# Kernel tuning notes

Measured on AMD Instinct MI355X. Metric: run time of the kernel, lower is better.

Reference implementation:

```python
import jax, jax.numpy as jnp
import numpy as np

SQ, SK, D = 8192, 8192, 128

def setup_inputs() -> dict:
    k = jax.random.key(0)
    kq, kk, kv = jax.random.split(k, 3)
    query = jax.random.normal(kq, (SQ, D), dtype=jnp.float32)
    key = jax.random.normal(kk, (SK, D), dtype=jnp.float32)
    value = jax.random.normal(kv, (SK, D), dtype=jnp.float32)
    return {"query": query, "key": key, "value": value}

def reference(query, key, value):
    # attn_weights = dot_general(q, k, contract last dims) -> [Sq, Sk]
    attn_weights = jnp.einsum('qd,kd->qk', query, key)
    # softmax over key dims (second half of attn_weights dims)
    attn_weights = jax.nn.softmax(attn_weights, axis=-1)
    # dropout is identity: train=False -> deterministic
    # y = dot_general(attn_weights, value, contract key dims) -> [Sq, Dv]
    y = jnp.einsum('qk,kd->qd', attn_weights, value)
    return y
```

## Files before the change

kernel.cpp:

```cpp
#include <hip/hip_runtime.h>
#include <hip/hip_bf16.h>
#include <stdint.h>

#define SQ 8192
#define SK 8192
#define DH 128
#define NIT 32
#define L2E 1.4426950408889634f
#define CB 40.0f

typedef __attribute__((ext_vector_type(8))) _Float16 f16x8;
typedef __attribute__((ext_vector_type(8))) short bf16x8;
typedef __attribute__((ext_vector_type(16))) float f32x16;
typedef __attribute__((ext_vector_type(4))) short s16x4;
typedef __attribute__((ext_vector_type(4))) unsigned int u32x4;

__device__ __forceinline__ short f2h(float f) {
  _Float16 h = (_Float16)f;
  return __builtin_bit_cast(short, h);
}
__device__ __forceinline__ short f2bf(float f) {
  uint32_t u = __builtin_bit_cast(uint32_t, f);
  u = (u + 0x7FFFu + ((u >> 16) & 1u)) >> 16;
  return (short)u;
}

__device__ __forceinline__ void gl_lds16(const void* g, void* l) {
  __builtin_amdgcn_global_load_lds(
      (const __attribute__((address_space(1))) void*)g,
      (__attribute__((address_space(3))) void*)l, 16, 0, 0);
}

__global__ __launch_bounds__(256) void prep_kernel(const float* __restrict__ K,
                                                   const float* __restrict__ V,
                                                   short* __restrict__ Kimg,
                                                   short* __restrict__ Vimg) {
  __shared__ short T[32][136];
  const int tid = threadIdx.x;
  if (blockIdx.x < 256) {
    const int kb = blockIdx.x;
#pragma unroll
    for (int i = 0; i < 2; ++i) {
      int ci = i * 256 + tid;
      int kc = ci >> 6, lane = ci & 63;
      int key = kb * 32 + (lane & 31);
      int k0 = kc * 16 + (lane >> 5) * 8;
      const float* src = K + (size_t)key * DH + k0;
      float4 a = *(const float4*)src;
      float4 b = *(const float4*)(src + 4);
      s16x4 o0, o1;
      o0.x = f2h(a.x); o0.y = f2h(a.y); o0.z = f2h(a.z); o0.w = f2h(a.w);
      o1.x = f2h(b.x); o1.y = f2h(b.y); o1.z = f2h(b.z); o1.w = f2h(b.w);
      s16x4* dst = (s16x4*)(Kimg + (size_t)kb * 4096 + ci * 8);
      dst[0] = o0; dst[1] = o1;
    }
  } else {
    const int kb = blockIdx.x - 256;
#pragma unroll
    for (int i = 0; i < 4; ++i) {
      int fi = i * 256 + tid;
      int key = fi >> 5;
      int dc = (fi & 31) * 4;
      float4 v = ((const float4*)V)[(size_t)(kb * 32 + key) * (DH / 4) + (fi & 31)];
      T[key][dc + 0] = f2bf(v.x); T[key][dc + 1] = f2bf(v.y);
      T[key][dc + 2] = f2bf(v.z); T[key][dc + 3] = f2bf(v.w);
    }
    __syncthreads();
#pragma unroll
    for (int i = 0; i < 2; ++i) {
      int ci = i * 256 + tid;
      int lane = ci & 63;
      int g = ci >> 6;
      int dt = g & 3, ks = g >> 2;
      int base = ks * 16 + (lane >> 5) * 4;
      int d = dt * 32 + (lane & 31);
      s16x4 o0, o1;
      o0.x = T[base + 0][d]; o0.y = T[base + 1][d];
      o0.z = T[base + 2][d]; o0.w = T[base + 3][d];
      o1.x = T[base + 8][d]; o1.y = T[base + 9][d];
      o1.z = T[base + 10][d]; o1.w = T[base + 11][d];
      s16x4* dst = (s16x4*)(Vimg + (size_t)kb * 4096 + ci * 8);
      dst[0] = o0; dst[1] = o1;
    }
  }
}

__global__ __launch_bounds__(512, 2) void attn_fallback(const float* __restrict__ Q,
                                                        const short* __restrict__ Kimg,
                                                        const short* __restrict__ Vimg,
                                                        float* __restrict__ out) {
  __shared__ __align__(16) char smem[67584];
  const int tid = threadIdx.x;
  const int w = tid >> 6;
  const int lane = tid & 63;
  const int half = lane >> 5;
  const int l32 = lane & 31;
  const int qrow0 = blockIdx.x * 32;

  f16x8 qf[8];
  {
    const float* qp = Q + (size_t)(qrow0 + l32) * DH + half * 8;
#pragma unroll
    for (int kc = 0; kc < 8; ++kc) {
      float4 a = *(const float4*)(qp + kc * 16);
      float4 b = *(const float4*)(qp + kc * 16 + 4);
      f16x8 h;
      h[0] = (_Float16)a.x; h[1] = (_Float16)a.y; h[2] = (_Float16)a.z; h[3] = (_Float16)a.w;
      h[4] = (_Float16)b.x; h[5] = (_Float16)b.y; h[6] = (_Float16)b.z; h[7] = (_Float16)b.w;
      qf[kc] = h;
    }
  }

  f32x16 of[4];
#pragma unroll
  for (int dt = 0; dt < 4; ++dt)
#pragma unroll
    for (int c = 0; c < 16; ++c) of[dt][c] = 0.f;
  float l_lane = 0.f;

  f16x8 kf[8];
  bf16x8 vf[8];
  {
    const short* kp = Kimg + (size_t)w * 4096;
    const short* vp = Vimg + (size_t)w * 4096;
#pragma unroll
    for (int kc = 0; kc < 8; ++kc) kf[kc] = *(const f16x8*)(kp + kc * 512 + lane * 8);
#pragma unroll
    for (int g = 0; g < 8; ++g) vf[g] = *(const bf16x8*)(vp + g * 512 + lane * 8);
  }

  for (int t = 0; t < NIT; ++t) {
    f32x16 sacc;
#pragma unroll
    for (int c = 0; c < 16; ++c) sacc[c] = 0.f;
#pragma unroll
    for (int kc = 0; kc < 8; ++kc)
      sacc = __builtin_amdgcn_mfma_f32_32x32x16_f16(kf[kc], qf[kc], sacc, 0, 0, 0);

    if (t + 1 < NIT) {
      const short* kp = Kimg + (size_t)((t + 1) * 8 + w) * 4096;
#pragma unroll
      for (int kc = 0; kc < 8; ++kc) kf[kc] = *(const f16x8*)(kp + kc * 512 + lane * 8);
    }

    u32x4 pav0, pav1;
#pragma unroll
    for (int r = 0; r < 4; ++r) {
      float pA = __builtin_amdgcn_exp2f(fmaf(sacc[2 * r], L2E, -CB));
      float pB = __builtin_amdgcn_exp2f(fmaf(sacc[2 * r + 1], L2E, -CB));
      float pC = __builtin_amdgcn_exp2f(fmaf(sacc[8 + 2 * r], L2E, -CB));
      float pD = __builtin_amdgcn_exp2f(fmaf(sacc[8 + 2 * r + 1], L2E, -CB));
      l_lane += (pA + pB) + (pC + pD);
      uint32_t uA = __builtin_bit_cast(uint32_t, pA); uA += 0x7FFFu + ((uA >> 16) & 1u);
      uint32_t uB = __builtin_bit_cast(uint32_t, pB); uB += 0x7FFFu + ((uB >> 16) & 1u);
      uint32_t uC = __builtin_bit_cast(uint32_t, pC); uC += 0x7FFFu + ((uC >> 16) & 1u);
      uint32_t uD = __builtin_bit_cast(uint32_t, pD); uD += 0x7FFFu + ((uD >> 16) & 1u);
      pav0[r] = __builtin_amdgcn_perm(uB, uA, 0x07060302u);
      pav1[r] = __builtin_amdgcn_perm(uD, uC, 0x07060302u);
    }
    bf16x8 pa0 = __builtin_bit_cast(bf16x8, pav0);
    bf16x8 pa1 = __builtin_bit_cast(bf16x8, pav1);

#pragma unroll
    for (int dt = 0; dt < 4; ++dt) {
      of[dt] = __builtin_amdgcn_mfma_f32_32x32x16_bf16(pa0, vf[dt], of[dt], 0, 0, 0);
      of[dt] = __builtin_amdgcn_mfma_f32_32x32x16_bf16(pa1, vf[4 + dt], of[dt], 0, 0, 0);
    }

    if (t + 1 < NIT) {
      const short* vp = Vimg + (size_t)((t + 1) * 8 + w) * 4096;
#pragma unroll
      for (int g = 0; g < 8; ++g) vf[g] = *(const bf16x8*)(vp + g * 512 + lane * 8);
    }
  }

  float l_tot = l_lane + __shfl_xor(l_lane, 32);

  __syncthreads();
  float* mO = (float*)smem;
  float* R = mO + (w & 3) * 4224;
  if (w < 4) {
#pragma unroll
    for (int c = 0; c < 16; ++c) {
      const int row = (c & 3) + 8 * (c >> 2) + 4 * half;
      float* br = R + row * 132;
#pragma unroll
      for (int dt = 0; dt < 4; ++dt) br[dt * 32 + l32] = of[dt][c];
    }
    if (half == 0) R[l32 * 132 + 128] = l_tot;
  }
  __syncthreads();
  if (w >= 4) {
#pragma unroll
    for (int c = 0; c < 16; ++c) {
      const int row = (c & 3) + 8 * (c >> 2) + 4 * half;
      float* br = R + row * 132;
#pragma unroll
      for (int dt = 0; dt < 4; ++dt) br[dt * 32 + l32] += of[dt][c];
    }
    if (half == 0) R[l32 * 132 + 128] += l_tot;
  }
  __syncthreads();
  {
    const int row = tid >> 4;
    const int cg = tid & 15;
    float den = mO[row * 132 + 128] + mO[4224 + row * 132 + 128] +
                mO[8448 + row * 132 + 128] + mO[12672 + row * 132 + 128];
    float inv = 1.f / den;
    float4 s0 = {0.f, 0.f, 0.f, 0.f}, s1 = {0.f, 0.f, 0.f, 0.f};
#pragma unroll
    for (int rg = 0; rg < 4; ++rg) {
      const float* p = mO + rg * 4224 + row * 132 + cg * 8;
      float4 a = *(const float4*)p;
      float4 b = *(const float4*)(p + 4);
      s0.x += a.x; s0.y += a.y; s0.z += a.z; s0.w += a.w;
      s1.x += b.x; s1.y += b.y; s1.z += b.z; s1.w += b.w;
    }
    s0.x *= inv; s0.y *= inv; s0.z *= inv; s0.w *= inv;
    s1.x *= inv; s1.y *= inv; s1.z *= inv; s1.w *= inv;
    float* op = out + (size_t)(qrow0 + row) * DH + cg * 8;
    *(float4*)op = s0;
    *(float4*)(op + 4) = s1;
  }
}

__global__ __launch_bounds__(512, 2) void attn_split(const float* __restrict__ Q,
                                                     const short* __restrict__ Kimg,
                                                     const short* __restrict__ Vimg,
                                                     float* __restrict__ Oa,
                                                     float* __restrict__ Ob,
                                                     float* __restrict__ l0,
                                                     float* __restrict__ l1) {
  __shared__ __align__(16) char smem[131072];
  short* stg = (short*)smem;
  const int tid = threadIdx.x;
  const int w = tid >> 6;
  const int lane = tid & 63;
  const int half = lane >> 5;
  const int l32 = lane & 31;
  const int qh = w >> 2;
  const int ks = w & 3;
  const int qb = blockIdx.x >> 1;
  const int kh = blockIdx.x & 1;
  const int qrow0 = qb * 64 + qh * 32;
  const int kb0 = kh * 128;

  f16x8 qf[8];
  {
    const float* qp = Q + (size_t)(qrow0 + l32) * DH + half * 8;
#pragma unroll
    for (int kc = 0; kc < 8; ++kc) {
      float4 a = *(const float4*)(qp + kc * 16);
      float4 b = *(const float4*)(qp + kc * 16 + 4);
      f16x8 h;
      h[0] = (_Float16)a.x; h[1] = (_Float16)a.y; h[2] = (_Float16)a.z; h[3] = (_Float16)a.w;
      h[4] = (_Float16)b.x; h[5] = (_Float16)b.y; h[6] = (_Float16)b.z; h[7] = (_Float16)b.w;
      qf[kc] = h;
    }
  }

  f32x16 of[4];
#pragma unroll
  for (int dt = 0; dt < 4; ++dt)
#pragma unroll
    for (int c = 0; c < 16; ++c) of[dt][c] = 0.f;
  float l_lane = 0.f;

  const short* gsrc = (w < 4 ? Kimg : Vimg) + ((size_t)kb0 + ks) * 4096 + lane * 8;
  short* lbase = stg + ((w >= 4) ? 16384 : 0) + ks * 4096;

  auto STAGE = [&](int c, int t) {
    const short* g = gsrc + (size_t)t * 4 * 4096;
    short* l = lbase + c * 32768;
#pragma unroll
    for (int j = 0; j < 8; ++j)
      gl_lds16(g + j * 512, l + j * 512);
  };

  STAGE(0, 0);
  __syncthreads();
  int cur = 0;

  for (int t = 0; t < NIT; ++t) {
    const short* bk = stg + cur * 32768 + ks * 4096 + lane * 8;
    f16x8 kf[8];
#pragma unroll
    for (int kc = 0; kc < 8; ++kc) kf[kc] = *(const f16x8*)(bk + kc * 512);

    if (t + 1 < NIT) STAGE(cur ^ 1, t + 1);

    f32x16 sacc;
#pragma unroll
    for (int c = 0; c < 16; ++c) sacc[c] = 0.f;
#pragma unroll
    for (int kc = 0; kc < 8; ++kc)
      sacc = __builtin_amdgcn_mfma_f32_32x32x16_f16(kf[kc], qf[kc], sacc, 0, 0, 0);

    const short* bv = stg + cur * 32768 + 16384 + ks * 4096 + lane * 8;
    bf16x8 vf[8];
#pragma unroll
    for (int g2 = 0; g2 < 8; ++g2) vf[g2] = *(const bf16x8*)(bv + g2 * 512);

    u32x4 pav0, pav1;
#pragma unroll
    for (int r = 0; r < 4; ++r) {
      float pA = __builtin_amdgcn_exp2f(fmaf(sacc[2 * r], L2E, -CB));
      float pB = __builtin_amdgcn_exp2f(fmaf(sacc[2 * r + 1], L2E, -CB));
      float pC = __builtin_amdgcn_exp2f(fmaf(sacc[8 + 2 * r], L2E, -CB));
      float pD = __builtin_amdgcn_exp2f(fmaf(sacc[8 + 2 * r + 1], L2E, -CB));
      l_lane += (pA + pB) + (pC + pD);
      uint32_t uA = __builtin_bit_cast(uint32_t, pA); uA += 0x7FFFu + ((uA >> 16) & 1u);
      uint32_t uB = __builtin_bit_cast(uint32_t, pB); uB += 0x7FFFu + ((uB >> 16) & 1u);
      uint32_t uC = __builtin_bit_cast(uint32_t, pC); uC += 0x7FFFu + ((uC >> 16) & 1u);
      uint32_t uD = __builtin_bit_cast(uint32_t, pD); uD += 0x7FFFu + ((uD >> 16) & 1u);
      pav0[r] = __builtin_amdgcn_perm(uB, uA, 0x07060302u);
      pav1[r] = __builtin_amdgcn_perm(uD, uC, 0x07060302u);
    }
    bf16x8 pa0 = __builtin_bit_cast(bf16x8, pav0);
    bf16x8 pa1 = __builtin_bit_cast(bf16x8, pav1);

#pragma unroll
    for (int dt = 0; dt < 4; ++dt) {
      of[dt] = __builtin_amdgcn_mfma_f32_32x32x16_bf16(pa0, vf[dt], of[dt], 0, 0, 0);
      of[dt] = __builtin_amdgcn_mfma_f32_32x32x16_bf16(pa1, vf[4 + dt], of[dt], 0, 0, 0);
    }

    __syncthreads();
    cur ^= 1;
  }

  float l_tot = l_lane + __shfl_xor(l_lane, 32);

  __syncthreads();
  float* mO = (float*)smem;
  float* R = mO + (qh * 2 + (ks & 1)) * 4224;
  if (ks < 2) {
#pragma unroll
    for (int c = 0; c < 16; ++c) {
      const int row = (c & 3) + 8 * (c >> 2) + 4 * half;
      float* br = R + row * 132;
#pragma unroll
      for (int dt = 0; dt < 4; ++dt) br[dt * 32 + l32] = of[dt][c];
    }
    if (half == 0) R[l32 * 132 + 128] = l_tot;
  }
  __syncthreads();
  if (ks >= 2) {
#pragma unroll
    for (int c = 0; c < 16; ++c) {
      const int row = (c & 3) + 8 * (c >> 2) + 4 * half;
      float* br = R + row * 132;
#pragma unroll
      for (int dt = 0; dt < 4; ++dt) br[dt * 32 + l32] += of[dt][c];
    }
    if (half == 0) R[l32 * 132 + 128] += l_tot;
  }
  __syncthreads();
  {
    const int row = tid >> 3;
    const int cg = tid & 7;
    const int qh2 = row >> 5;
    const int r32 = row & 31;
    const float* Ra = mO + (qh2 * 2 + 0) * 4224 + r32 * 132;
    const float* Rb = mO + (qh2 * 2 + 1) * 4224 + r32 * 132;
    float lp = Ra[128] + Rb[128];
    float* dst = (kh ? Ob : Oa) + (size_t)(qb * 64 + row) * DH + cg * 16;
#pragma unroll
    for (int k = 0; k < 4; ++k) {
      float4 a = *(const float4*)(Ra + cg * 16 + k * 4);
      float4 b = *(const float4*)(Rb + cg * 16 + k * 4);
      a.x += b.x; a.y += b.y; a.z += b.z; a.w += b.w;
      *(float4*)(dst + k * 4) = a;
    }
    if (cg == 0) (kh ? l1 : l0)[qb * 64 + row] = lp;
  }
}

__global__ __launch_bounds__(256) void combine_kernel(float* __restrict__ Oa,
                                                      const float* __restrict__ Ob,
                                                      const float* __restrict__ l0,
                                                      const float* __restrict__ l1) {
  const int idx = blockIdx.x * 256 + threadIdx.x;
  const int row = idx >> 5;
  const int c4 = (idx & 31) * 4;
  const float inv = 1.f / (l0[row] + l1[row]);
  float* pa = Oa + (size_t)row * DH + c4;
  const float* pb = Ob + (size_t)row * DH + c4;
  float4 a = *(const float4*)pa;
  float4 b = *(const float4*)pb;
  a.x = (a.x + b.x) * inv; a.y = (a.y + b.y) * inv;
  a.z = (a.z + b.z) * inv; a.w = (a.w + b.w) * inv;
  *(float4*)pa = a;
}

extern "C" void kernel_launch(void* const* d_in, const int* in_sizes, int n_in,
                              void* d_out, int out_size, void* d_ws, size_t ws_size,
                              hipStream_t stream) {
  const float* Q = (const float*)d_in[0];
  const float* K = (const float*)d_in[1];
  const float* V = (const float*)d_in[2];
  float* out = (float*)d_out;
  char* ws = (char*)d_ws;
  short* Kimg = (short*)ws;
  short* Vimg = (short*)(ws + 2097152);
  prep_kernel<<<512, 256, 0, stream>>>(K, V, Kimg, Vimg);
  if (ws_size >= (size_t)8454144) {
    float* Ob = (float*)(ws + 4194304);
    float* l0 = (float*)(ws + 8388608);
    float* l1 = l0 + SQ;
    attn_split<<<SQ / 64 * 2, 512, 0, stream>>>(Q, Kimg, Vimg, out, Ob, l0, l1);
    combine_kernel<<<SQ * DH / 4 / 256, 256, 0, stream>>>(out, Ob, l0, l1);
  } else {
    attn_fallback<<<SQ / 32, 512, 0, stream>>>(Q, Kimg, Vimg, out);
  }
}
```

Measured before the change: 112.9 us.

## Add 128-query-row attention kernel with 4-way key split and triple-buffered LDS

Adds a new primary path where each block handles 128 query rows across 8 waves and a quarter of the keys. K/V tiles are staged into LDS with a 3-deep async pipeline, so each staged tile is reused by four query groups instead of two. A four-way combine kernel merges the partial outputs and denominators. The old split kernel becomes the fallback when the workspace is too small. In exchange the path needs a larger workspace and writes four partial output arrays, which adds global traffic and an extra reduction.

```diff
diff --git a/kernel.cpp b/kernel.cpp
--- a/kernel.cpp
+++ b/kernel.cpp
@@ -5,7 +5,6 @@
 #define SQ 8192
 #define SK 8192
 #define DH 128
-#define NIT 32
 #define L2E 1.4426950408889634f
 #define CB 40.0f
 
@@ -85,17 +84,26 @@
   }
 }
 
-__global__ __launch_bounds__(512, 2) void attn_fallback(const float* __restrict__ Q,
-                                                        const short* __restrict__ Kimg,
-                                                        const short* __restrict__ Vimg,
-                                                        float* __restrict__ out) {
-  __shared__ __align__(16) char smem[67584];
+#define NIT4 32
+__global__ __launch_bounds__(512, 2) void attn_q128(const float* __restrict__ Q,
+                                                    const short* __restrict__ Kimg,
+                                                    const short* __restrict__ Vimg,
+                                                    float* __restrict__ Opart,
+                                                    float* __restrict__ lpart) {
+  __shared__ __align__(16) char smem[98304];
+  short* stg = (short*)smem;
   const int tid = threadIdx.x;
   const int w = tid >> 6;
   const int lane = tid & 63;
   const int half = lane >> 5;
   const int l32 = lane & 31;
-  const int qrow0 = blockIdx.x * 32;
+  const int qh = w >> 1;
+  const int kw = w & 1;
+  const int b = blockIdx.x;
+  const int kh = b & 3;
+  const int qb = b >> 2;
+  const int qrow0 = qb * 128 + qh * 32;
+  const int kb0 = kh * 64;
 
   f16x8 qf[8];
   {
@@ -103,10 +111,10 @@
 #pragma unroll
     for (int kc = 0; kc < 8; ++kc) {
       float4 a = *(const float4*)(qp + kc * 16);
-      float4 b = *(const float4*)(qp + kc * 16 + 4);
+      float4 b2 = *(const float4*)(qp + kc * 16 + 4);
       f16x8 h;
       h[0] = (_Float16)a.x; h[1] = (_Float16)a.y; h[2] = (_Float16)a.z; h[3] = (_Float16)a.w;
-      h[4] = (_Float16)b.x; h[5] = (_Float16)b.y; h[6] = (_Float16)b.z; h[7] = (_Float16)b.w;
+      h[4] = (_Float16)b2.x; h[5] = (_Float16)b2.y; h[6] = (_Float16)b2.z; h[7] = (_Float16)b2.w;
       qf[kc] = h;
     }
   }
@@ -118,18 +126,32 @@
     for (int c = 0; c < 16; ++c) of[dt][c] = 0.f;
   float l_lane = 0.f;
 
-  f16x8 kf[8];
-  bf16x8 vf[8];
-  {
-    const short* kp = Kimg + (size_t)w * 4096;
-    const short* vp = Vimg + (size_t)w * 4096;
-#pragma unroll
-    for (int kc = 0; kc < 8; ++kc) kf[kc] = *(const f16x8*)(kp + kc * 512 + lane * 8);
-#pragma unroll
-    for (int g = 0; g < 8; ++g) vf[g] = *(const bf16x8*)(vp + g * 512 + lane * 8);
-  }
-
-  for (int t = 0; t < NIT; ++t) {
+  const short* gsrc = (w < 4 ? Kimg : Vimg) + (size_t)kb0 * 4096 + (w & 3) * 2048 + lane * 8;
+  const int ldso = ((w < 4) ? 0 : 8192) + (w & 3) * 2048;
+
+  auto STAGE = [&](int c, int t) {
+    const short* g = gsrc + (size_t)t * 8192;
+    short* l = stg + c * 16384 + ldso;
+#pragma unroll
+    for (int j = 0; j < 4; ++j)
+      gl_lds16(g + j * 512, l + j * 512);
+  };
+
+  STAGE(0, 0);
+  STAGE(1, 1);
+  asm volatile("s_waitcnt vmcnt(4)" ::: "memory");
+  __builtin_amdgcn_s_barrier();
+  __builtin_amdgcn_sched_barrier(0);
+
+  for (int t = 0; t < NIT4; ++t) {
+    const int cur = t % 3;
+    const short* bk = stg + cur * 16384 + kw * 4096 + lane * 8;
+    f16x8 kf[8];
+#pragma unroll
+    for (int kc = 0; kc < 8; ++kc) kf[kc] = *(const f16x8*)(bk + kc * 512);
+
+    if (t + 2 < NIT4) STAGE((t + 2) % 3, t + 2);
+
     f32x16 sacc;
 #pragma unroll
     for (int c = 0; c < 16; ++c) sacc[c] = 0.f;
@@ -137,11 +159,10 @@
     for (int kc = 0; kc < 8; ++kc)
       sacc = __builtin_amdgcn_mfma_f32_32x32x16_f16(kf[kc], qf[kc], sacc, 0, 0, 0);
 
-    if (t + 1 < NIT) {
-      const short* kp = Kimg + (size_t)((t + 1) * 8 + w) * 4096;
-#pragma unroll
-      for (int kc = 0; kc < 8; ++kc) kf[kc] = *(const f16x8*)(kp + kc * 512 + lane * 8);
-    }
+    const short* bv = stg + cur * 16384 + 8192 + kw * 4096 + lane * 8;
+    bf16x8 vf[8];
+#pragma unroll
+    for (int g2 = 0; g2 < 8; ++g2) vf[g2] = *(const bf16x8*)(bv + g2 * 512);
 
     u32x4 pav0, pav1;
 #pragma unroll
@@ -167,10 +188,10 @@
       of[dt] = __builtin_amdgcn_mfma_f32_32x32x16_bf16(pa1, vf[4 + dt], of[dt], 0, 0, 0);
     }
 
-    if (t + 1 < NIT) {
-      const short* vp = Vimg + (size_t)((t + 1) * 8 + w) * 4096;
-#pragma unroll
-      for (int g = 0; g < 8; ++g) vf[g] = *(const bf16x8*)(vp + g * 512 + lane * 8);
+    if (t + 1 < NIT4) {
+      asm volatile("s_waitcnt vmcnt(4)" ::: "memory");
+      __builtin_amdgcn_s_barrier();
+      __builtin_amdgcn_sched_barrier(0);
     }
   }
 
@@ -178,8 +199,8 @@
 
   __syncthreads();
   float* mO = (float*)smem;
-  float* R = mO + (w & 3) * 4224;
-  if (w < 4) {
+  float* R = mO + qh * 4224;
+  if (kw == 0) {
 #pragma unroll
     for (int c = 0; c < 16; ++c) {
       const int row = (c & 3) + 8 * (c >> 2) + 4 * half;
@@ -190,7 +211,7 @@
     if (half == 0) R[l32 * 132 + 128] = l_tot;
   }
   __syncthreads();
-  if (w >= 4) {
+  if (kw == 1) {
 #pragma unroll
     for (int c = 0; c < 16; ++c) {
       const int row = (c & 3) + 8 * (c >> 2) + 4 * half;
@@ -202,35 +223,44 @@
   }
   __syncthreads();
   {
-    const int row = tid >> 4;
-    const int cg = tid & 15;
-    float den = mO[row * 132 + 128] + mO[4224 + row * 132 + 128] +
-                mO[8448 + row * 132 + 128] + mO[12672 + row * 132 + 128];
-    float inv = 1.f / den;
-    float4 s0 = {0.f, 0.f, 0.f, 0.f}, s1 = {0.f, 0.f, 0.f, 0.f};
-#pragma unroll
-    for (int rg = 0; rg < 4; ++rg) {
-      const float* p = mO + rg * 4224 + row * 132 + cg * 8;
-      float4 a = *(const float4*)p;
-      float4 b = *(const float4*)(p + 4);
-      s0.x += a.x; s0.y += a.y; s0.z += a.z; s0.w += a.w;
-      s1.x += b.x; s1.y += b.y; s1.z += b.z; s1.w += b.w;
-    }
-    s0.x *= inv; s0.y *= inv; s0.z *= inv; s0.w *= inv;
-    s1.x *= inv; s1.y *= inv; s1.z *= inv; s1.w *= inv;
-    float* op = out + (size_t)(qrow0 + row) * DH + cg * 8;
-    *(float4*)op = s0;
-    *(float4*)(op + 4) = s1;
-  }
-}
-
-__global__ __launch_bounds__(512, 2) void attn_split(const float* __restrict__ Q,
-                                                     const short* __restrict__ Kimg,
-                                                     const short* __restrict__ Vimg,
-                                                     float* __restrict__ Oa,
-                                                     float* __restrict__ Ob,
-                                                     float* __restrict__ l0,
-                                                     float* __restrict__ l1) {
+    const int row = tid >> 2;
+    const int cg = tid & 3;
+    const float* p = mO + (row >> 5) * 4224 + (row & 31) * 132;
+    float* dst = Opart + ((size_t)kh << 20) + (size_t)(qb * 128 + row) * DH + cg * 32;
+#pragma unroll
+    for (int k = 0; k < 8; ++k)
+      ((float4*)dst)[k] = ((const float4*)(p + cg * 32))[k];
+    if (cg == 0) lpart[kh * SQ + qb * 128 + row] = p[128];
+  }
+}
+
+__global__ __launch_bounds__(256) void combine4(const float* __restrict__ Opart,
+                                                const float* __restrict__ lpart,
+                                                float* __restrict__ out) {
+  const int idx = blockIdx.x * 256 + threadIdx.x;
+  const int row = idx >> 5;
+  const int c4 = (idx & 31) * 4;
+  const float inv = 1.f / (lpart[row] + lpart[SQ + row] +
+                           lpart[2 * SQ + row] + lpart[3 * SQ + row]);
+  const size_t off = (size_t)row * DH + c4;
+  float4 a = *(const float4*)(Opart + off);
+  const float4 b = *(const float4*)(Opart + (1u << 20) + off);
+  const float4 c = *(const float4*)(Opart + (2u << 20) + off);
+  const float4 d = *(const float4*)(Opart + (3u << 20) + off);
+  a.x = (a.x + b.x + c.x + d.x) * inv;
+  a.y = (a.y + b.y + c.y + d.y) * inv;
+  a.z = (a.z + b.z + c.z + d.z) * inv;
+  a.w = (a.w + b.w + c.w + d.w) * inv;
+  *(float4*)(out + off) = a;
+}
+
+__global__ __launch_bounds__(512, 2) void attn_fb(const float* __restrict__ Q,
+                                                  const short* __restrict__ Kimg,
+                                                  const short* __restrict__ Vimg,
+                                                  float* __restrict__ Oa,
+                                                  float* __restrict__ Ob,
+                                                  float* __restrict__ l0,
+                                                  float* __restrict__ l1) {
   __shared__ __align__(16) char smem[131072];
   short* stg = (short*)smem;
   const int tid = threadIdx.x;
@@ -281,13 +311,13 @@
   __syncthreads();
   int cur = 0;
 
-  for (int t = 0; t < NIT; ++t) {
-    const short* bk = stg + cur * 32768 + ks * 4096 + lane * 8;
+  for (int t = 0; t < 32; ++t) {
+    const short* bk = stg + cur * 16384 * 2 + ks * 4096 + lane * 8;
     f16x8 kf[8];
 #pragma unroll
     for (int kc = 0; kc < 8; ++kc) kf[kc] = *(const f16x8*)(bk + kc * 512);
 
-    if (t + 1 < NIT) STAGE(cur ^ 1, t + 1);
+    if (t + 1 < 32) STAGE(cur ^ 1, t + 1);
 
     f32x16 sacc;
 #pragma unroll
@@ -296,7 +326,7 @@
     for (int kc = 0; kc < 8; ++kc)
       sacc = __builtin_amdgcn_mfma_f32_32x32x16_f16(kf[kc], qf[kc], sacc, 0, 0, 0);
 
-    const short* bv = stg + cur * 32768 + 16384 + ks * 4096 + lane * 8;
+    const short* bv = stg + cur * 16384 * 2 + 16384 + ks * 4096 + lane * 8;
     bf16x8 vf[8];
 #pragma unroll
     for (int g2 = 0; g2 < 8; ++g2) vf[g2] = *(const bf16x8*)(bv + g2 * 512);
@@ -376,10 +406,10 @@
   }
 }
 
-__global__ __launch_bounds__(256) void combine_kernel(float* __restrict__ Oa,
-                                                      const float* __restrict__ Ob,
-                                                      const float* __restrict__ l0,
-                                                      const float* __restrict__ l1) {
+__global__ __launch_bounds__(256) void combine2(float* __restrict__ Oa,
+                                                const float* __restrict__ Ob,
+                                                const float* __restrict__ l0,
+                                                const float* __restrict__ l1) {
   const int idx = blockIdx.x * 256 + threadIdx.x;
   const int row = idx >> 5;
   const int c4 = (idx & 31) * 4;
@@ -404,13 +434,16 @@
   short* Kimg = (short*)ws;
   short* Vimg = (short*)(ws + 2097152);
   prep_kernel<<<512, 256, 0, stream>>>(K, V, Kimg, Vimg);
-  if (ws_size >= (size_t)8454144) {
+  if (ws_size >= (size_t)21102592) {
+    float* Opart = (float*)(ws + 4194304);
+    float* lpart = (float*)(ws + 20971520);
+    attn_q128<<<256, 512, 0, stream>>>(Q, Kimg, Vimg, Opart, lpart);
+    combine4<<<SQ * DH / 4 / 256, 256, 0, stream>>>(Opart, lpart, out);
+  } else {
     float* Ob = (float*)(ws + 4194304);
     float* l0 = (float*)(ws + 8388608);
     float* l1 = l0 + SQ;
-    attn_split<<<SQ / 64 * 2, 512, 0, stream>>>(Q, Kimg, Vimg, out, Ob, l0, l1);
-    combine_kernel<<<SQ * DH / 4 / 256, 256, 0, stream>>>(out, Ob, l0, l1);
-  } else {
-    attn_fallback<<<SQ / 32, 512, 0, stream>>>(Q, Kimg, Vimg, out);
-  }
-}
+    attn_fb<<<SQ / 64 * 2, 512, 0, stream>>>(Q, Kimg, Vimg, out, Ob, l0, l1);
+    combine2<<<SQ * DH / 4 / 256, 256, 0, stream>>>(out, Ob, l0, l1);
+  }
+}
```

New measurement: 115.2 us. About the same (+2.0%).
